# Performance work log

Hardware: AMD Instinct MI355X
Metric: run time of the kernel (lower is better)

The kernel has to match this reference:

```python
import jax, jax.numpy as jnp
import numpy as np
from jax import lax

# Dimensions (must match input_specs)
B, T, C = 2, 2048, 1024
H = 4 * C          # FFN hidden
E_RWKV, E_TRANS = 6, 2
E = E_RWKV + E_TRANS
LN_EPS = 1e-5


def layernorm(x, g, b):
    m = x.mean(-1, keepdims=True)
    v = ((x - m) ** 2).mean(-1, keepdims=True)
    return (x - m) * lax.rsqrt(v + LN_EPS) * g + b


def setup_inputs() -> dict:
    key = jax.random.key(0)
    ks = jax.random.split(key, 24)
    s = 0.02
    inp = {
        "x": jax.random.normal(ks[0], (B, T, C), jnp.float32),
        "v_first": jax.random.normal(ks[1], (B, T, C), jnp.float32),
        "winners": jax.random.randint(ks[2], (B, T, 2), 0, E),
        "capital_shares": jax.random.uniform(ks[3], (E,), jnp.float32),
        # LayerNorms
        "ln1_g": jnp.ones((C,), jnp.float32), "ln1_b": jnp.zeros((C,), jnp.float32),
        "ln2_g": jnp.ones((C,), jnp.float32), "ln2_b": jnp.zeros((C,), jnp.float32),
        # RWKV-style time-mix (simplified RWKV7_TimeMix)
        "Wr": s * jax.random.normal(ks[4], (C, C), jnp.float32),
        "Wk": s * jax.random.normal(ks[5], (C, C), jnp.float32),
        "Wv": s * jax.random.normal(ks[6], (C, C), jnp.float32),
        "Wo": s * jax.random.normal(ks[7], (C, C), jnp.float32),
        "w_decay": jax.random.normal(ks[8], (C,), jnp.float32),
        "g_v": jax.random.normal(ks[9], (C,), jnp.float32),
        # bridge: linear on concat(h, rwkv_state)
        "Wb": s * jax.random.normal(ks[10], (2 * C, C), jnp.float32),
        "bb": jnp.zeros((C,), jnp.float32),
        # 6 stacked SparseRWKVFFN experts: sigmoid(x Wr_r) * (relu(x Wk_r)^2 Wv_r)
        "Wk_r": s * jax.random.normal(ks[11], (E_RWKV, C, H), jnp.float32),
        "Wv_r": s * jax.random.normal(ks[12], (E_RWKV, H, C), jnp.float32),
        "Wr_r": s * jax.random.normal(ks[13], (E_RWKV, C, C), jnp.float32),
        # 2 stacked LinearTransformerExpert: gelu((h+prefix) W1) W2
        "W1_t": s * jax.random.normal(ks[14], (E_TRANS, C, H), jnp.float32),
        "W2_t": s * jax.random.normal(ks[15], (E_TRANS, H, C), jnp.float32),
    }
    return inp


def reference(x, v_first, winners, capital_shares,
              ln1_g, ln1_b, ln2_g, ln2_b,
              Wr, Wk, Wv, Wo, w_decay, g_v,
              Wb, bb, Wk_r, Wv_r, Wr_r, W1_t, W2_t):
    # ---- attention (simplified RWKV time-mix), returns per-token state ----
    h1 = layernorm(x, ln1_g, ln1_b)
    r = jax.nn.sigmoid(h1 @ Wr)                      # [B,T,C]
    k = h1 @ Wk
    v = h1 @ Wv
    v = v + (v_first - v) * jax.nn.sigmoid(g_v)      # value-residual mix
    w = jax.nn.sigmoid(w_decay)                      # per-channel decay [C]

    def step(s, kv):
        k_t, v_t = kv                                # [B,C] each
        s = w * s + k_t * v_t
        return s, s

    s0 = jnp.zeros((B, C), x.dtype)
    _, states = lax.scan(step, s0, (jnp.swapaxes(k, 0, 1), jnp.swapaxes(v, 0, 1)))
    states = jnp.swapaxes(states, 0, 1)              # rwkv_state [B,T,C]

    att_out = (r * states) @ Wo
    x = x + att_out
    h = layernorm(x, ln2_g, ln2_b)

    # ---- bridge prefix (flat over tokens, vectorized) ----
    bridge_prefix = jnp.concatenate([h, states], axis=-1) @ Wb + bb  # [B,T,C]

    # ---- experts computed densely, combined by top-2 gates ----
    # RWKV FFN experts
    a = jnp.square(jax.nn.relu(jnp.einsum('btc,ech->ebth', h, Wk_r)))     # [Er,B,T,H]
    rec = jax.nn.sigmoid(jnp.einsum('btc,ecd->ebtd', h, Wr_r))            # [Er,B,T,C]
    out_r = rec * jnp.einsum('ebth,ehc->ebtc', a, Wv_r)                   # [Er,B,T,C]
    # Linear-transformer experts consume the bridge prefix
    ht = h + bridge_prefix
    out_t = jnp.einsum('ebth,ehc->ebtc',
                       jax.nn.gelu(jnp.einsum('btc,ech->ebth', ht, W1_t)),
                       W2_t)                                              # [Et,B,T,C]
    all_out = jnp.concatenate([out_r, out_t], axis=0)                     # [E,B,T,C]

    # top-2 combine, each rank weighted 0.5 (use_market=False branch)
    gate = 0.5 * (jax.nn.one_hot(winners[..., 0], E, dtype=x.dtype)
                  + jax.nn.one_hot(winners[..., 1], E, dtype=x.dtype))    # [B,T,E]
    final_out = jnp.einsum('ebtc,bte->btc', all_out, gate)

    return x + final_out
```

## Files before the change

kernel.cpp:

```cpp
#include <hip/hip_runtime.h>

typedef unsigned short u16;
typedef __bf16 bf16x8 __attribute__((ext_vector_type(8)));
typedef float f32x4 __attribute__((ext_vector_type(4)));

__device__ __forceinline__ float bf2f(u16 u){ union{unsigned i;float f;}x; x.i=((unsigned)u)<<16; return x.f; }
__device__ __forceinline__ u16 f2bf(float f){ union{float f;unsigned i;}x; x.f=f; unsigned r = x.i + 0x7FFFu + ((x.i>>16)&1u); return (u16)(r>>16); }
__device__ __forceinline__ float sigm(float x){ return 1.f/(1.f+expf(-x)); }

struct __align__(8) U16x4 { u16 v[4]; };

#define PSTRIDE 8388608ull

struct CJob { const float* src; u16* dst; int K, N, base; };
struct CJobs { CJob j[27]; };

__global__ void conv_all(CJobs cj){
  __shared__ u16 tile[128][65];
  int id = blockIdx.x;
  int sel = 0;
  #pragma unroll
  for (int i=1;i<27;++i) if (cj.j[i].base <= id) sel = i;
  const float* __restrict__ src = cj.j[sel].src;
  u16* __restrict__ dst = cj.j[sel].dst;
  int K = cj.j[sel].K, N = cj.j[sel].N;
  int lt = id - cj.j[sel].base;
  int tn = N >> 6;
  int k0 = (lt / tn) * 128, n0 = (lt % tn) * 64;
  int tid = threadIdx.x;
  #pragma unroll
  for (int it=0; it<8; ++it){
    int e = it*1024 + tid*4;
    int r = e>>6, c = e&63;
    float4 v = *(const float4*)(src + (size_t)(k0+r)*N + n0 + c);
    tile[r][c+0]=f2bf(v.x); tile[r][c+1]=f2bf(v.y); tile[r][c+2]=f2bf(v.z); tile[r][c+3]=f2bf(v.w);
  }
  __syncthreads();
  #pragma unroll
  for (int it=0; it<8; ++it){
    int e = it*1024 + tid*4;
    int n = e>>7, k = e&127;
    U16x4 o;
    #pragma unroll
    for (int j=0;j<4;++j) o.v[j] = tile[k+j][n];
    *(U16x4*)(dst + (size_t)(n0+n)*K + k0 + k) = o;
  }
}

__global__ void ln_k(const float* __restrict__ x, const float* __restrict__ g, const float* __restrict__ b,
                     u16* __restrict__ out, int ostride){
  int row = blockIdx.x, tid = threadIdx.x;
  float4 v = *(const float4*)(x + (size_t)row*1024 + tid*4);
  float s = v.x+v.y+v.z+v.w;
  float ss = v.x*v.x+v.y*v.y+v.z*v.z+v.w*v.w;
  #pragma unroll
  for (int o=32;o;o>>=1){ s += __shfl_down(s,o); ss += __shfl_down(ss,o); }
  __shared__ float sm[8];
  int lane = tid&63, wv = tid>>6;
  if (!lane){ sm[wv]=s; sm[4+wv]=ss; }
  __syncthreads();
  s = sm[0]+sm[1]+sm[2]+sm[3]; ss = sm[4]+sm[5]+sm[6]+sm[7];
  float mean = s*(1.f/1024.f);
  float var = ss*(1.f/1024.f) - mean*mean;
  float inv = rsqrtf(var + 1e-5f);
  U16x4 o;
  const float* vp = &v.x;
  #pragma unroll
  for (int j=0;j<4;++j){
    int c = tid*4+j;
    o.v[j] = f2bf((vp[j]-mean)*inv*g[c] + b[c]);
  }
  *(U16x4*)(out + (size_t)row*ostride + tid*4) = o;
}

__global__ void red_x_ln(const float* __restrict__ x, const u16* __restrict__ part,
                         const float* __restrict__ g, const float* __restrict__ b,
                         float* __restrict__ out, u16* __restrict__ hcat){
  int row = blockIdx.x, tid = threadIdx.x;
  size_t i = (size_t)row*1024 + tid*4;
  U16x4 p0 = *(const U16x4*)(part + i);
  U16x4 p1 = *(const U16x4*)(part + PSTRIDE + i);
  float4 xv = *(const float4*)(x + i);
  float4 v;
  v.x = xv.x + bf2f(p0.v[0]) + bf2f(p1.v[0]);
  v.y = xv.y + bf2f(p0.v[1]) + bf2f(p1.v[1]);
  v.z = xv.z + bf2f(p0.v[2]) + bf2f(p1.v[2]);
  v.w = xv.w + bf2f(p0.v[3]) + bf2f(p1.v[3]);
  *(float4*)(out + i) = v;
  float s = v.x+v.y+v.z+v.w;
  float ss = v.x*v.x+v.y*v.y+v.z*v.z+v.w*v.w;
  #pragma unroll
  for (int o=32;o;o>>=1){ s += __shfl_down(s,o); ss += __shfl_down(ss,o); }
  __shared__ float sm[8];
  int lane = tid&63, wv = tid>>6;
  if (!lane){ sm[wv]=s; sm[4+wv]=ss; }
  __syncthreads();
  s = sm[0]+sm[1]+sm[2]+sm[3]; ss = sm[4]+sm[5]+sm[6]+sm[7];
  float mean = s*(1.f/1024.f);
  float var = ss*(1.f/1024.f) - mean*mean;
  float inv = rsqrtf(var + 1e-5f);
  U16x4 o;
  const float* vp = &v.x;
  #pragma unroll
  for (int j=0;j<4;++j){
    int c = tid*4+j;
    o.v[j] = f2bf((vp[j]-mean)*inv*g[c] + b[c]);
  }
  *(U16x4*)(hcat + (size_t)row*2048 + tid*4) = o;
}

__global__ void scan_p1(const u16* __restrict__ kbuf, const u16* __restrict__ vbuf,
                        const float* __restrict__ w_decay, float* __restrict__ carry){
  int c = blockIdx.x*256 + threadIdx.x;
  int chunk = blockIdx.y, b = blockIdx.z;
  float w = sigm(w_decay[c]);
  float s = 0.f;
  size_t idx = ((size_t)(b*2048 + chunk*64))*1024 + c;
  #pragma unroll 4
  for (int i=0;i<64;++i){ s = w*s + bf2f(kbuf[idx])*bf2f(vbuf[idx]); idx += 1024; }
  carry[((size_t)(b*32+chunk))*1024 + c] = s;
}
__global__ void scan_p2(const float* __restrict__ w_decay, const float* __restrict__ carry,
                        float* __restrict__ startv){
  int c = blockIdx.x*256 + threadIdx.x;
  int b = blockIdx.y;
  float w = sigm(w_decay[c]);
  float wL = w;
  #pragma unroll
  for (int i=0;i<6;++i) wL *= wL;
  float p = 0.f;
  for (int j=0;j<32;++j){
    size_t id = ((size_t)(b*32+j))*1024 + c;
    startv[id] = p;
    p = wL*p + carry[id];
  }
}
__global__ void scan_p3(const u16* __restrict__ kbuf, const u16* __restrict__ vbuf, const u16* __restrict__ rbuf,
                        const float* __restrict__ w_decay, const float* __restrict__ startv,
                        u16* __restrict__ rs, u16* __restrict__ hcat){
  int c = blockIdx.x*256 + threadIdx.x;
  int chunk = blockIdx.y, b = blockIdx.z;
  float w = sigm(w_decay[c]);
  float s = startv[((size_t)(b*32+chunk))*1024 + c];
  size_t t0 = (size_t)b*2048 + chunk*64;
  size_t idx = t0*1024 + c;
  size_t idx2 = t0*2048 + 1024 + c;
  for (int i=0;i<64;++i){
    s = w*s + bf2f(kbuf[idx])*bf2f(vbuf[idx]);
    rs[idx] = f2bf(bf2f(rbuf[idx]) * s);
    hcat[idx2] = f2bf(s);
    idx += 1024; idx2 += 2048;
  }
}

__global__ void route_count(const int* __restrict__ winners, int* __restrict__ offs, int* __restrict__ cursor){
  __shared__ int cnt[8];
  if (threadIdx.x < 8) cnt[threadIdx.x] = 0;
  __syncthreads();
  for (int p = threadIdx.x; p < 8192; p += 256) atomicAdd(&cnt[winners[p]&7], 1);
  __syncthreads();
  if (threadIdx.x == 0){
    int s = 0;
    #pragma unroll
    for (int e=0;e<8;++e){ offs[e]=s; s+=cnt[e]; }
    offs[8]=s;
  }
  if (threadIdx.x < 8) cursor[threadIdx.x] = 0;
}
__global__ void route_scatter(const int* __restrict__ winners, const int* __restrict__ offs,
                              int* __restrict__ cursor, int* __restrict__ idx_all){
  int p = blockIdx.x*256 + threadIdx.x;
  if (p < 8192){
    int e = winners[p]&7;
    int pos = offs[e] + atomicAdd(&cursor[e], 1);
    idx_all[pos] = p>>1;
  }
}


struct GArgs {
  const u16* A; const u16* B;
  long long lda, bstride;
  int K, Mdense, eBase, nxt, kdiv;
  const int* offs; const int* idx_all;
  const float* v_first; const float* g_v;
  u16* rbuf; u16* kbuf; u16* vbuf;
  u16* act; u16* part;
};

#define GLL(gp, lp) __builtin_amdgcn_global_load_lds((const __attribute__((address_space(1))) void*)(gp), \
                                                     (__attribute__((address_space(3))) void*)(lp), 16, 0, 0)

template<int EPI, int GATHER>
__global__ __launch_bounds__(256,3) void gemm_k(GArgs g){
  int e = g.eBase + blockIdx.z;
  int rbase = 0, m = g.Mdense;
  if (g.offs){ rbase = g.offs[e]; m = g.offs[e+1] - rbase; }
  if ((int)blockIdx.y * 128 >= m) return;
  const int xt = (int)blockIdx.x % g.nxt;
  const int ksplit = (int)blockIdx.x / g.nxt;
  const long long kOff = (long long)ksplit * g.kdiv;
  __shared__ char smem[49152];
  const int tid = threadIdx.x, lane = tid&63, wave = tid>>6;
  const int wr = wave>>1, wc = wave&1;
  const int nk = g.kdiv >> 5;

  const int srowi = tid>>2;
  const long long scol = (long long)((((tid&3) ^ ((tid>>3)&3)))*8);

  const u16* bBase0 = g.B + (long long)blockIdx.z*g.bstride
                    + ((long long)(xt*128) + srowi)*(long long)g.K + kOff + scol;
  const u16* bBase1 = bBase0 + 64ll*(long long)g.K;

  const int sw = ((lane>>4) ^ ((lane>>1)&3)) << 4;
  int aRd[4], bRd[4];
  #pragma unroll
  for (int q=0;q<4;++q){
    aRd[q] = (wr*64 + q*16 + (lane&15))*64 + sw;
    bRd[q] = 8192 + (wc*64 + q*16 + (lane&15))*64 + sw;
  }

  for (int mt = blockIdx.y; mt*128 < m; mt += gridDim.y){
    const u16 *aP0, *aP1;
    {
      int g0 = mt*128 + srowi;       g0 = g0 < m ? g0 : m-1;
      int g1 = mt*128 + 64 + srowi;  g1 = g1 < m ? g1 : m-1;
      long long r0, r1;
      if (GATHER){ r0 = g.idx_all[rbase+g0]; r1 = g.idx_all[rbase+g1]; }
      else if (g.offs){ r0 = rbase+g0; r1 = rbase+g1; }
      else { r0 = g0; r1 = g1; }
      aP0 = g.A + r0*g.lda + kOff + scol;
      aP1 = g.A + r1*g.lda + kOff + scol;
    }
    const u16* bP0 = bBase0;
    const u16* bP1 = bBase1;

    f32x4 acc[4][4];
    #pragma unroll
    for (int mm=0;mm<4;++mm)
      #pragma unroll
      for (int nn=0;nn<4;++nn)
        acc[mm][nn] = f32x4{0.f,0.f,0.f,0.f};

    #define STAGE(BUF) do{ \
      char* db = smem + (BUF)*16384 + wave*1024; \
      GLL(aP0, db); GLL(aP1, db+4096); GLL(bP0, db+8192); GLL(bP1, db+12288); \
      aP0+=32; aP1+=32; bP0+=32; bP1+=32; }while(0)

    STAGE(0); STAGE(1);
    int bufC = 0, bufS = 2;
    for (int ks=0; ks<nk; ++ks){
      if (ks+2 < nk){
        STAGE(bufS); bufS = bufS==2 ? 0 : bufS+1;
        asm volatile("s_waitcnt vmcnt(8)" ::: "memory");
      } else if (ks+1 < nk){
        asm volatile("s_waitcnt vmcnt(4)" ::: "memory");
      } else {
        asm volatile("s_waitcnt vmcnt(0)" ::: "memory");
      }
      asm volatile("s_barrier" ::: "memory");
      const char* base = smem + bufC*16384;
      bf16x8 af[4], bfv[4];
      #pragma unroll
      for (int q=0;q<4;++q) af[q] = *(const bf16x8*)(base + aRd[q]);
      #pragma unroll
      for (int q=0;q<4;++q) bfv[q] = *(const bf16x8*)(base + bRd[q]);
      #pragma unroll
      for (int mm=0;mm<4;++mm)
        #pragma unroll
        for (int nn=0;nn<4;++nn)
          acc[mm][nn] = __builtin_amdgcn_mfma_f32_16x16x32_bf16(af[mm], bfv[nn], acc[mm][nn], 0,0,0);
      asm volatile("s_waitcnt lgkmcnt(0)" ::: "memory");
      asm volatile("s_barrier" ::: "memory");
      bufC = bufC==2 ? 0 : bufC+1;
    }
    #undef STAGE

    int colB = xt*128 + wc*64 + (lane&15);
    #pragma unroll
    for (int mm=0;mm<4;++mm){
      #pragma unroll
      for (int j=0;j<4;++j){
        int grow = mt*128 + wr*64 + mm*16 + (lane>>4)*4 + j;
        if (grow >= m) continue;
        size_t gr = (size_t)(rbase + grow);
        #pragma unroll
        for (int nn=0;nn<4;++nn){
          int col = colB + nn*16;
          float val = acc[mm][nn][j];
          if (EPI==0){
            if (col < 1024) g.rbuf[gr*1024+col] = f2bf(sigm(val));
            else if (col < 2048) g.kbuf[gr*1024+col-1024] = f2bf(val);
            else {
              int c2 = col-2048;
              float sg = sigm(g.g_v[c2]);
              float vf = g.v_first[gr*1024+c2];
              g.vbuf[gr*1024+c2] = f2bf(val + (vf-val)*sg);
            }
          } else {
            g.part[(size_t)ksplit*PSTRIDE + gr*1024 + col] = f2bf(val);
          }
        }
      }
    }
  }
}

struct MoeArgs {
  const u16* hcat; const u16* htb; const u16* act;
  const u16* wTkr; const u16* wT1; const u16* wTrr; const u16* wTvr; const u16* wT2;
  const int* offs; const int* idx_all;
  u16* actw; u16* part;
};

template<int PHASE>
__global__ __launch_bounds__(256,3) void gemm_moe(MoeArgs g){
  const int T  = (int)(gridDim.x*gridDim.y*gridDim.z);
  const int id = (int)(blockIdx.x + gridDim.x*(blockIdx.y + gridDim.y*blockIdx.z));
  const int work = (id&7)*(T>>3) + (id>>3);
  const int bx = work % (int)gridDim.x;
  const int rest = work / (int)gridDim.x;
  const int by = rest % (int)gridDim.y;
  const int z  = rest / (int)gridDim.y;

  const u16 *Ap, *Bp; long long lda; int K, kdiv, nxt, e, epi;
  if (PHASE==0){
    if (z < 6){ e=z;   Ap=g.hcat; lda=2048; Bp=g.wTkr + (long long)z*4096*1024;     K=1024; kdiv=1024; nxt=32; epi=0; }
    else if (z < 8){ e=z; Ap=g.htb; lda=1024; Bp=g.wT1 + (long long)(z-6)*4096*1024; K=1024; kdiv=1024; nxt=32; epi=1; }
    else { e=z-8; Ap=g.hcat; lda=2048; Bp=g.wTrr + (long long)(z-8)*1024*1024;      K=1024; kdiv=512;  nxt=8;  epi=2; }
  } else {
    if (z < 6){ e=z; Ap=g.act; lda=4096; Bp=g.wTvr + (long long)z*1024*4096;        K=4096; kdiv=2048; nxt=8;  epi=3; }
    else { e=z;     Ap=g.act; lda=4096; Bp=g.wT2 + (long long)(z-6)*1024*4096;      K=4096; kdiv=1024; nxt=8;  epi=4; }
  }
  if (bx >= nxt * (K / kdiv)) return;
  int rbase = g.offs[e], m = g.offs[e+1] - rbase;
  if (by * 128 >= m) return;
  const int xt = bx % nxt;
  const int ksplit = bx / nxt;
  const long long kOff = (long long)ksplit * kdiv;
  __shared__ char smem[49152];
  const int tid = threadIdx.x, lane = tid&63, wave = tid>>6;
  const int wr = wave>>1, wc = wave&1;
  const int nk = kdiv >> 5;

  const int srowi = tid>>2;
  const long long scol = (long long)((((tid&3) ^ ((tid>>3)&3)))*8);

  const u16* bBase0 = Bp + ((long long)(xt*128) + srowi)*(long long)K + kOff + scol;
  const u16* bBase1 = bBase0 + 64ll*(long long)K;

  const int sw = ((lane>>4) ^ ((lane>>1)&3)) << 4;
  int aRd[4], bRd[4];
  #pragma unroll
  for (int q=0;q<4;++q){
    aRd[q] = (wr*64 + q*16 + (lane&15))*64 + sw;
    bRd[q] = 8192 + (wc*64 + q*16 + (lane&15))*64 + sw;
  }

  for (int mt = by; mt*128 < m; mt += gridDim.y){
    const u16 *aP0, *aP1;
    {
      int g0 = mt*128 + srowi;       g0 = g0 < m ? g0 : m-1;
      int g1 = mt*128 + 64 + srowi;  g1 = g1 < m ? g1 : m-1;
      long long r0, r1;
      if (epi <= 2){ r0 = g.idx_all[rbase+g0]; r1 = g.idx_all[rbase+g1]; }
      else { r0 = rbase+g0; r1 = rbase+g1; }
      aP0 = Ap + r0*lda + kOff + scol;
      aP1 = Ap + r1*lda + kOff + scol;
    }
    const u16* bP0 = bBase0;
    const u16* bP1 = bBase1;

    f32x4 acc[4][4];
    #pragma unroll
    for (int mm=0;mm<4;++mm)
      #pragma unroll
      for (int nn=0;nn<4;++nn)
        acc[mm][nn] = f32x4{0.f,0.f,0.f,0.f};

    #define STAGE(BUF) do{ \
      char* db = smem + (BUF)*16384 + wave*1024; \
      GLL(aP0, db); GLL(aP1, db+4096); GLL(bP0, db+8192); GLL(bP1, db+12288); \
      aP0+=32; aP1+=32; bP0+=32; bP1+=32; }while(0)

    STAGE(0); STAGE(1);
    int bufC = 0, bufS = 2;
    for (int ks=0; ks<nk; ++ks){
      if (ks+2 < nk){
        STAGE(bufS); bufS = bufS==2 ? 0 : bufS+1;
        asm volatile("s_waitcnt vmcnt(8)" ::: "memory");
      } else if (ks+1 < nk){
        asm volatile("s_waitcnt vmcnt(4)" ::: "memory");
      } else {
        asm volatile("s_waitcnt vmcnt(0)" ::: "memory");
      }
      asm volatile("s_barrier" ::: "memory");
      const char* base = smem + bufC*16384;
      bf16x8 af[4], bfv[4];
      #pragma unroll
      for (int q=0;q<4;++q) af[q] = *(const bf16x8*)(base + aRd[q]);
      #pragma unroll
      for (int q=0;q<4;++q) bfv[q] = *(const bf16x8*)(base + bRd[q]);
      #pragma unroll
      for (int mm=0;mm<4;++mm)
        #pragma unroll
        for (int nn=0;nn<4;++nn)
          acc[mm][nn] = __builtin_amdgcn_mfma_f32_16x16x32_bf16(af[mm], bfv[nn], acc[mm][nn], 0,0,0);
      asm volatile("s_waitcnt lgkmcnt(0)" ::: "memory");
      asm volatile("s_barrier" ::: "memory");
      bufC = bufC==2 ? 0 : bufC+1;
    }
    #undef STAGE

    int colB = xt*128 + wc*64 + (lane&15);
    #pragma unroll
    for (int mm=0;mm<4;++mm){
      #pragma unroll
      for (int j=0;j<4;++j){
        int grow = mt*128 + wr*64 + mm*16 + (lane>>4)*4 + j;
        if (grow >= m) continue;
        size_t gr = (size_t)(rbase + grow);
        #pragma unroll
        for (int nn=0;nn<4;++nn){
          int col = colB + nn*16;
          float val = acc[mm][nn][j];
          if (epi == 0){
            float r_ = fmaxf(val, 0.f);
            g.actw[gr*4096+col] = f2bf(r_*r_);
          } else if (epi == 1){
            float t3 = val*val*val;
            float th = tanhf(0.79788456080286535588f*(val + 0.044715f*t3));
            g.actw[gr*4096+col] = f2bf(0.5f*val*(1.f+th));
          } else if (epi == 2){
            g.part[(size_t)(2+ksplit)*PSTRIDE + gr*1024 + col] = f2bf(val);
          } else {
            g.part[(size_t)ksplit*PSTRIDE + gr*1024 + col] = f2bf(val);
          }
        }
      }
    }
  }
}

__global__ void red_ht(const u16* __restrict__ hcat, const u16* __restrict__ part,
                       const float* __restrict__ bb, u16* __restrict__ ht){
  int c = threadIdx.x*4;
  size_t i = (size_t)blockIdx.x*1024 + c;
  U16x4 p0 = *(const U16x4*)(part + i);
  U16x4 p1 = *(const U16x4*)(part + PSTRIDE + i);
  U16x4 hv = *(const U16x4*)(hcat + (size_t)blockIdx.x*2048 + c);
  U16x4 o;
  #pragma unroll
  for (int j=0;j<4;++j) o.v[j] = f2bf(bf2f(hv.v[j]) + bf2f(p0.v[j]) + bf2f(p1.v[j]) + bb[c+j]);
  *(U16x4*)(ht + i) = o;
}
__global__ void red_moe(const int* __restrict__ offs, const int* __restrict__ idx_all,
                        const u16* __restrict__ part, float* __restrict__ out){
  int gr = blockIdx.x;
  if (gr >= offs[8]) return;
  int tok = idx_all[gr];
  bool isr = gr < offs[6];
  int c = threadIdx.x*4;
  size_t i = (size_t)gr*1024 + c;
  U16x4 p0 = *(const U16x4*)(part + i);
  U16x4 p1 = *(const U16x4*)(part + PSTRIDE + i);
  U16x4 p2 = *(const U16x4*)(part + 2*PSTRIDE + i);
  U16x4 p3 = *(const U16x4*)(part + 3*PSTRIDE + i);
  #pragma unroll
  for (int j=0;j<4;++j){
    float v;
    if (isr){
      float rc = sigm(bf2f(p2.v[j]) + bf2f(p3.v[j]));
      v = 0.5f*(bf2f(p0.v[j]) + bf2f(p1.v[j]))*rc;
    } else {
      v = 0.5f*(bf2f(p0.v[j]) + bf2f(p1.v[j]) + bf2f(p2.v[j]) + bf2f(p3.v[j]));
    }
    atomicAdd(&out[(size_t)tok*1024 + c + j], v);
  }
}

extern "C" void kernel_launch(void* const* d_in, const int* in_sizes, int n_in,
                              void* d_out, int out_size, void* d_ws, size_t ws_size,
                              hipStream_t stream) {
  const float* x       = (const float*)d_in[0];
  const float* v_first = (const float*)d_in[1];
  const int*   winners = (const int*)d_in[2];
  const float* ln1_g   = (const float*)d_in[4];
  const float* ln1_b   = (const float*)d_in[5];
  const float* ln2_g   = (const float*)d_in[6];
  const float* ln2_b   = (const float*)d_in[7];
  const float* Wr      = (const float*)d_in[8];
  const float* Wk      = (const float*)d_in[9];
  const float* Wv      = (const float*)d_in[10];
  const float* Wo      = (const float*)d_in[11];
  const float* w_decay = (const float*)d_in[12];
  const float* g_v     = (const float*)d_in[13];
  const float* Wb      = (const float*)d_in[14];
  const float* bb      = (const float*)d_in[15];
  const float* Wk_r    = (const float*)d_in[16];
  const float* Wv_r    = (const float*)d_in[17];
  const float* Wr_r    = (const float*)d_in[18];
  const float* W1_t    = (const float*)d_in[19];
  const float* W2_t    = (const float*)d_in[20];
  float* out = (float*)d_out;

  char* p = (char*)d_ws;
  auto alloc = [&](size_t bytes)->char*{ char* r=p; p += (bytes+255)&~(size_t)255; return r; };
  u16* wTrkv = (u16*)alloc(3072ull*1024*2);
  u16* wTo   = (u16*)alloc(1024ull*1024*2);
  u16* wTb   = (u16*)alloc(1024ull*2048*2);
  u16* wTkr  = (u16*)alloc(6ull*4096*1024*2);
  u16* wTvr  = (u16*)alloc(6ull*1024*4096*2);
  u16* wTrr  = (u16*)alloc(6ull*1024*1024*2);
  u16* wT1   = (u16*)alloc(2ull*4096*1024*2);
  u16* wT2   = (u16*)alloc(2ull*1024*4096*2);
  u16* h1    = (u16*)alloc(4096ull*1024*2);
  u16* rbuf  = (u16*)alloc(4096ull*1024*2);
  u16* kbuf  = (u16*)alloc(4096ull*1024*2);
  u16* vbuf  = (u16*)alloc(4096ull*1024*2);
  u16* rsb   = (u16*)alloc(4096ull*1024*2);
  u16* hcat  = (u16*)alloc(4096ull*2048*2);
  u16* htb   = (u16*)alloc(4096ull*1024*2);
  u16* act   = (u16*)alloc(8192ull*4096*2);
  u16* partial = (u16*)alloc(4ull*8192*1024*2);
  float* carry  = (float*)alloc(2ull*32*1024*4);
  float* startv = (float*)alloc(2ull*32*1024*4);
  int* offs   = (int*)alloc(16*4);
  int* cursor = (int*)alloc(8*4);
  int* idx_all= (int*)alloc(8192*4);

  dim3 B256(256);

  {
    CJobs cj; int base = 0, ji = 0;
    auto add = [&](const float* s, u16* d, int K, int N){
      cj.j[ji++] = CJob{s, d, K, N, base}; base += (K>>7)*(N>>6);
    };
    add(Wr, wTrkv, 1024,1024); add(Wk, wTrkv+1024*1024, 1024,1024);
    add(Wv, wTrkv+2048*1024, 1024,1024); add(Wo, wTo, 1024,1024);
    add(Wb, wTb, 2048,1024);
    for (int e2=0;e2<6;++e2) add(Wk_r + (size_t)e2*1024*4096, wTkr + (size_t)e2*4096*1024, 1024,4096);
    for (int e2=0;e2<6;++e2) add(Wv_r + (size_t)e2*4096*1024, wTvr + (size_t)e2*1024*4096, 4096,1024);
    for (int e2=0;e2<6;++e2) add(Wr_r + (size_t)e2*1024*1024, wTrr + (size_t)e2*1024*1024, 1024,1024);
    for (int e2=0;e2<2;++e2) add(W1_t + (size_t)e2*1024*4096, wT1 + (size_t)e2*4096*1024, 1024,4096);
    for (int e2=0;e2<2;++e2) add(W2_t + (size_t)e2*4096*1024, wT2 + (size_t)e2*1024*4096, 4096,1024);
    conv_all<<<dim3(base,1,1),B256,0,stream>>>(cj);
  }

  route_count<<<1,B256,0,stream>>>(winners, offs, cursor);
  route_scatter<<<32,B256,0,stream>>>(winners, offs, cursor, idx_all);

  ln_k<<<4096,B256,0,stream>>>(x, ln1_g, ln1_b, h1, 1024);

  {
    GArgs ga{}; ga.A=h1; ga.B=wTrkv; ga.lda=1024; ga.K=1024; ga.Mdense=4096; ga.nxt=24; ga.kdiv=1024;
    ga.v_first=v_first; ga.g_v=g_v; ga.rbuf=rbuf; ga.kbuf=kbuf; ga.vbuf=vbuf;
    gemm_k<0,0><<<dim3(24,32,1),B256,0,stream>>>(ga);
  }

  scan_p1<<<dim3(4,32,2),B256,0,stream>>>(kbuf, vbuf, w_decay, carry);
  scan_p2<<<dim3(4,2,1), B256,0,stream>>>(w_decay, carry, startv);
  scan_p3<<<dim3(4,32,2),B256,0,stream>>>(kbuf, vbuf, rbuf, w_decay, startv, rsb, hcat);

  {
    GArgs ga{}; ga.A=rsb; ga.B=wTo; ga.lda=1024; ga.K=1024; ga.Mdense=4096; ga.nxt=8; ga.kdiv=512;
    ga.part=partial;
    gemm_k<1,0><<<dim3(16,32,1),B256,0,stream>>>(ga);
  }
  red_x_ln<<<4096,B256,0,stream>>>(x, partial, ln2_g, ln2_b, out, hcat);

  {
    GArgs ga{}; ga.A=hcat; ga.B=wTb; ga.lda=2048; ga.K=2048; ga.Mdense=4096; ga.nxt=8; ga.kdiv=1024;
    ga.part=partial;
    gemm_k<2,0><<<dim3(16,32,1),B256,0,stream>>>(ga);
  }
  red_ht<<<4096,B256,0,stream>>>(hcat, partial, bb, htb);

  {
    MoeArgs ma{};
    ma.hcat=hcat; ma.htb=htb; ma.act=act;
    ma.wTkr=wTkr; ma.wT1=wT1; ma.wTrr=wTrr; ma.wTvr=wTvr; ma.wT2=wT2;
    ma.offs=offs; ma.idx_all=idx_all; ma.actw=act; ma.part=partial;
    gemm_moe<0><<<dim3(32,6,14),B256,0,stream>>>(ma);
    gemm_moe<1><<<dim3(32,6,8),B256,0,stream>>>(ma);
  }
  red_moe<<<8192,B256,0,stream>>>(offs, idx_all, partial, out);

  (void)in_sizes; (void)n_in; (void)out_size; (void)ws_size;
}
```

Measured before the change: 712.6 us.

## Overlap expert weight conversion with scan kernels; widen MoE grid y

Splits the single fp32→bf16 weight-transpose launch into a small upfront part (attention and bridge weights) plus two expert-weight batches. The batches run as extra blocks appended to the latency-bound, low-occupancy scan phase-1 and phase-3 kernels, so conversion bandwidth overlaps the sequential scan work. The MoE GEMM grid y dimension also grows from 6 to 8, which only helps if the kernel uses the extra blocks, for example under tail-based expert indexing. Risks include scan blocks being slowed by competing conversion blocks, and the grid change altering expert coverage or adding empty blocks.

```diff
diff --git a/kernel.cpp b/kernel.cpp
--- a/kernel.cpp
+++ b/kernel.cpp
@@ -15,9 +15,7 @@
 struct CJob { const float* src; u16* dst; int K, N, base; };
 struct CJobs { CJob j[27]; };
 
-__global__ void conv_all(CJobs cj){
-  __shared__ u16 tile[128][65];
-  int id = blockIdx.x;
+__device__ __forceinline__ void conv_tile(const CJobs& cj, int id, u16 (*tile)[65]){
   int sel = 0;
   #pragma unroll
   for (int i=1;i<27;++i) if (cj.j[i].base <= id) sel = i;
@@ -45,6 +43,11 @@
     for (int j=0;j<4;++j) o.v[j] = tile[k+j][n];
     *(U16x4*)(dst + (size_t)(n0+n)*K + k0 + k) = o;
   }
+}
+
+__global__ void conv_all(CJobs cj){
+  __shared__ u16 tile[128][65];
+  conv_tile(cj, blockIdx.x, tile);
 }
 
 __global__ void ln_k(const float* __restrict__ x, const float* __restrict__ g, const float* __restrict__ b,
@@ -109,16 +112,22 @@
   *(U16x4*)(hcat + (size_t)row*2048 + tid*4) = o;
 }
 
-__global__ void scan_p1(const u16* __restrict__ kbuf, const u16* __restrict__ vbuf,
-                        const float* __restrict__ w_decay, float* __restrict__ carry){
-  int c = blockIdx.x*256 + threadIdx.x;
-  int chunk = blockIdx.y, b = blockIdx.z;
-  float w = sigm(w_decay[c]);
-  float s = 0.f;
-  size_t idx = ((size_t)(b*2048 + chunk*64))*1024 + c;
-  #pragma unroll 4
-  for (int i=0;i<64;++i){ s = w*s + bf2f(kbuf[idx])*bf2f(vbuf[idx]); idx += 1024; }
-  carry[((size_t)(b*32+chunk))*1024 + c] = s;
+__global__ void scan1_conv(const u16* __restrict__ kbuf, const u16* __restrict__ vbuf,
+                           const float* __restrict__ w_decay, float* __restrict__ carry, CJobs cj){
+  __shared__ u16 tile[128][65];
+  int id = blockIdx.x;
+  if (id < 256){
+    int c = (id&3)*256 + threadIdx.x;
+    int chunk = (id>>2)&31, b = id>>7;
+    float w = sigm(w_decay[c]);
+    float s = 0.f;
+    size_t idx = ((size_t)(b*2048 + chunk*64))*1024 + c;
+    #pragma unroll 4
+    for (int i=0;i<64;++i){ s = w*s + bf2f(kbuf[idx])*bf2f(vbuf[idx]); idx += 1024; }
+    carry[((size_t)(b*32+chunk))*1024 + c] = s;
+    return;
+  }
+  conv_tile(cj, id - 256, tile);
 }
 __global__ void scan_p2(const float* __restrict__ w_decay, const float* __restrict__ carry,
                         float* __restrict__ startv){
@@ -135,22 +144,28 @@
     p = wL*p + carry[id];
   }
 }
-__global__ void scan_p3(const u16* __restrict__ kbuf, const u16* __restrict__ vbuf, const u16* __restrict__ rbuf,
-                        const float* __restrict__ w_decay, const float* __restrict__ startv,
-                        u16* __restrict__ rs, u16* __restrict__ hcat){
-  int c = blockIdx.x*256 + threadIdx.x;
-  int chunk = blockIdx.y, b = blockIdx.z;
-  float w = sigm(w_decay[c]);
-  float s = startv[((size_t)(b*32+chunk))*1024 + c];
-  size_t t0 = (size_t)b*2048 + chunk*64;
-  size_t idx = t0*1024 + c;
-  size_t idx2 = t0*2048 + 1024 + c;
-  for (int i=0;i<64;++i){
-    s = w*s + bf2f(kbuf[idx])*bf2f(vbuf[idx]);
-    rs[idx] = f2bf(bf2f(rbuf[idx]) * s);
-    hcat[idx2] = f2bf(s);
-    idx += 1024; idx2 += 2048;
-  }
+__global__ void scan3_conv(const u16* __restrict__ kbuf, const u16* __restrict__ vbuf, const u16* __restrict__ rbuf,
+                           const float* __restrict__ w_decay, const float* __restrict__ startv,
+                           u16* __restrict__ rs, u16* __restrict__ hcat, CJobs cj){
+  __shared__ u16 tile[128][65];
+  int id = blockIdx.x;
+  if (id < 256){
+    int c = (id&3)*256 + threadIdx.x;
+    int chunk = (id>>2)&31, b = id>>7;
+    float w = sigm(w_decay[c]);
+    float s = startv[((size_t)(b*32+chunk))*1024 + c];
+    size_t t0 = (size_t)b*2048 + chunk*64;
+    size_t idx = t0*1024 + c;
+    size_t idx2 = t0*2048 + 1024 + c;
+    for (int i=0;i<64;++i){
+      s = w*s + bf2f(kbuf[idx])*bf2f(vbuf[idx]);
+      rs[idx] = f2bf(bf2f(rbuf[idx]) * s);
+      hcat[idx2] = f2bf(s);
+      idx += 1024; idx2 += 2048;
+    }
+    return;
+  }
+  conv_tile(cj, id - 256, tile);
 }
 
 __global__ void route_count(const int* __restrict__ winners, int* __restrict__ offs, int* __restrict__ cursor){
@@ -531,20 +546,41 @@
 
   dim3 B256(256);
 
+  auto pad = [](CJobs& cj, int ji){ for (; ji<27; ++ji) cj.j[ji] = CJob{nullptr,nullptr,0,0,0x7FFFFFFF}; };
+
+  CJobs cjS; int baseS = 0;
   {
-    CJobs cj; int base = 0, ji = 0;
+    int ji = 0;
     auto add = [&](const float* s, u16* d, int K, int N){
-      cj.j[ji++] = CJob{s, d, K, N, base}; base += (K>>7)*(N>>6);
+      cjS.j[ji++] = CJob{s, d, K, N, baseS}; baseS += (K>>7)*(N>>6);
     };
     add(Wr, wTrkv, 1024,1024); add(Wk, wTrkv+1024*1024, 1024,1024);
     add(Wv, wTrkv+2048*1024, 1024,1024); add(Wo, wTo, 1024,1024);
     add(Wb, wTb, 2048,1024);
+    pad(cjS, ji);
+  }
+  conv_all<<<dim3(baseS,1,1),B256,0,stream>>>(cjS);
+
+  CJobs cjE1; int baseE1 = 0;
+  {
+    int ji = 0;
+    auto add = [&](const float* s, u16* d, int K, int N){
+      cjE1.j[ji++] = CJob{s, d, K, N, baseE1}; baseE1 += (K>>7)*(N>>6);
+    };
     for (int e2=0;e2<6;++e2) add(Wk_r + (size_t)e2*1024*4096, wTkr + (size_t)e2*4096*1024, 1024,4096);
+    for (int e2=0;e2<6;++e2) add(Wr_r + (size_t)e2*1024*1024, wTrr + (size_t)e2*1024*1024, 1024,1024);
+    pad(cjE1, ji);
+  }
+  CJobs cjE2; int baseE2 = 0;
+  {
+    int ji = 0;
+    auto add = [&](const float* s, u16* d, int K, int N){
+      cjE2.j[ji++] = CJob{s, d, K, N, baseE2}; baseE2 += (K>>7)*(N>>6);
+    };
     for (int e2=0;e2<6;++e2) add(Wv_r + (size_t)e2*4096*1024, wTvr + (size_t)e2*1024*4096, 4096,1024);
-    for (int e2=0;e2<6;++e2) add(Wr_r + (size_t)e2*1024*1024, wTrr + (size_t)e2*1024*1024, 1024,1024);
     for (int e2=0;e2<2;++e2) add(W1_t + (size_t)e2*1024*4096, wT1 + (size_t)e2*4096*1024, 1024,4096);
     for (int e2=0;e2<2;++e2) add(W2_t + (size_t)e2*4096*1024, wT2 + (size_t)e2*1024*4096, 4096,1024);
-    conv_all<<<dim3(base,1,1),B256,0,stream>>>(cj);
+    pad(cjE2, ji);
   }
 
   route_count<<<1,B256,0,stream>>>(winners, offs, cursor);
@@ -558,9 +594,9 @@
     gemm_k<0,0><<<dim3(24,32,1),B256,0,stream>>>(ga);
   }
 
-  scan_p1<<<dim3(4,32,2),B256,0,stream>>>(kbuf, vbuf, w_decay, carry);
+  scan1_conv<<<dim3(256+baseE1,1,1),B256,0,stream>>>(kbuf, vbuf, w_decay, carry, cjE1);
   scan_p2<<<dim3(4,2,1), B256,0,stream>>>(w_decay, carry, startv);
-  scan_p3<<<dim3(4,32,2),B256,0,stream>>>(kbuf, vbuf, rbuf, w_decay, startv, rsb, hcat);
+  scan3_conv<<<dim3(256+baseE2,1,1),B256,0,stream>>>(kbuf, vbuf, rbuf, w_decay, startv, rsb, hcat, cjE2);
 
   {
     GArgs ga{}; ga.A=rsb; ga.B=wTo; ga.lda=1024; ga.K=1024; ga.Mdense=4096; ga.nxt=8; ga.kdiv=512;
@@ -581,8 +617,8 @@
     ma.hcat=hcat; ma.htb=htb; ma.act=act;
     ma.wTkr=wTkr; ma.wT1=wT1; ma.wTrr=wTrr; ma.wTvr=wTvr; ma.wT2=wT2;
     ma.offs=offs; ma.idx_all=idx_all; ma.actw=act; ma.part=partial;
-    gemm_moe<0><<<dim3(32,6,14),B256,0,stream>>>(ma);
-    gemm_moe<1><<<dim3(32,6,8),B256,0,stream>>>(ma);
+    gemm_moe<0><<<dim3(32,8,14),B256,0,stream>>>(ma);
+    gemm_moe<1><<<dim3(32,8,8),B256,0,stream>>>(ma);
   }
   red_moe<<<8192,B256,0,stream>>>(offs, idx_all, partial, out);
 
```

Measured after the change: 706.8 us. Within noise of the previous version (-0.8%).
